# Kernel tuning notes

Measured on AMD Instinct MI355X. Metric: run time of the kernel, lower is better.

## Reference

```python
import jax, jax.numpy as jnp
import numpy as np

# Module constants from init_kwargs
DIM = 3      # qudit dimension
NQ = 15      # number of qudits
INDEX = 7    # target qudit -> esq = INDEX qudits left, dir = NQ-INDEX-1 right
J, K = 0, 1  # generalized sigma_x levels
D = DIM ** NQ


def setup_inputs() -> dict:
    key = jax.random.key(0)
    k1, k2, k3 = jax.random.split(key, 3)
    x_real = jax.random.normal(k1, (D, 1), dtype=jnp.float32)
    x_imag = jax.random.normal(k2, (D, 1), dtype=jnp.float32)
    angle = jax.random.normal(k3, (1,), dtype=jnp.float32)
    return {"x_real": x_real, "x_imag": x_imag, "angle": angle}


def reference(x_real, x_imag, angle):
    # Generator S = |j><k| + |k><j| (generalized sigma_x, mtx_id=0)
    S = jnp.zeros((DIM, DIM), dtype=jnp.complex64).at[J, K].set(1.0).at[K, J].set(1.0)
    # M = expm(-0.5i * angle * S), a tiny DIMxDIM unitary
    M = jax.scipy.linalg.expm((-0.5j) * angle[0].astype(jnp.complex64) * S)
    # State vector: complex amplitudes
    x = jax.lax.complex(x_real, x_imag)  # (D, 1) complex64
    d_left = DIM ** INDEX
    d_right = DIM ** (NQ - INDEX - 1)
    # (I_left kron M kron I_right) @ x == contract M on the middle qudit axis
    xr = x.reshape(d_left, DIM, d_right)
    y = jnp.einsum('ij,ajb->aib', M, xr)
    return y.reshape(D, 1)
```

## Files before the change

### kernel.cpp

```cpp
#include <hip/hip_runtime.h>
#include <hip/hip_bf16.h>


constexpr int DR = 2187;
constexpr int ROWSTRIDE = 3 * DR;
constexpr int NPAIRS = 4782969;

__global__ __launch_bounds__(256) void rot_kernel(
    const float* __restrict__ xr,
    const float* __restrict__ xi,
    const float* __restrict__ angle,
    __hip_bfloat162* __restrict__ out)
{
    int p = blockIdx.x * blockDim.x + threadIdx.x;
    if (p >= NPAIRS) return;

    float half = 0.5f * angle[0];
    float s = sinf(half);
    float c = cosf(half);

    int a = p / DR;
    int b = p - a * DR;
    int base = a * ROWSTRIDE + b;

    float x0r = xr[base],          x0i = xi[base];
    float x1r = xr[base + DR],     x1i = xi[base + DR];
    float x2r = xr[base + 2 * DR], x2i = xi[base + 2 * DR];

    float y0r = c * x0r + s * x1i;
    float y0i = c * x0i - s * x1r;
    float y1r = s * x0i + c * x1r;
    float y1i = c * x1i - s * x0r;

    __hip_bfloat162 o0, o1, o2;
    o0.x = __float2bfloat16(y0i); o0.y = __float2bfloat16(y0r);
    o1.x = __float2bfloat16(y1i); o1.y = __float2bfloat16(y1r);
    o2.x = __float2bfloat16(x2i); o2.y = __float2bfloat16(x2r);

    out[base]          = o0;
    out[base + DR]     = o1;
    out[base + 2 * DR] = o2;
}

extern "C" void kernel_launch(void* const* d_in, const int* in_sizes, int n_in,
                              void* d_out, int out_size, void* d_ws, size_t ws_size,
                              hipStream_t stream) {
    const float* big[2] = {nullptr, nullptr};
    const float* angle = nullptr;
    int nbig = 0;
    for (int i = 0; i < n_in; ++i) {
        if (in_sizes[i] == 1) angle = (const float*)d_in[i];
        else if (nbig < 2)    big[nbig++] = (const float*)d_in[i];
    }
    const float* xr = big[0];
    const float* xi = big[1];
    __hip_bfloat162* out = (__hip_bfloat162*)d_out;

    const int block = 256;
    const int grid = (NPAIRS + block - 1) / block;
    rot_kernel<<<grid, block, 0, stream>>>(xr, xi, angle, out);
}
```

Measured before the change: 32.74 us.

## Stage row planes in LDS with float4 loads and vectorize passthrough plane

Each block now handles one left index row: the first two qudit planes are loaded with float4 vector loads into shared memory, and the untouched third plane is copied straight to output with float4 loads and packed 128-bit stores. The rotation then reads partner elements from LDS. This replaces scalar strided per-thread loads and the per-element divide with wide coalesced transfers, at the cost of a block-wide barrier, about 35KB of LDS per block, and alignment prologue/epilogue handling.

```diff
diff --git a/kernel.cpp b/kernel.cpp
--- a/kernel.cpp
+++ b/kernel.cpp
@@ -2,44 +2,100 @@
 #include <hip/hip_bf16.h>
 
 
-constexpr int DR = 2187;
-constexpr int ROWSTRIDE = 3 * DR;
-constexpr int NPAIRS = 4782969;
+constexpr int PLANE = 2187;
+constexpr int TWO_PLANES = 4374;
+constexpr int ROWLEN = 6561;
+constexpr int NROWS = 2187;
 
-__global__ __launch_bounds__(256) void rot_kernel(
+__device__ __forceinline__ uint32_t pack_bf2(float re, float im) {
+    __hip_bfloat162 h;
+    h.x = __float2bfloat16(im);
+    h.y = __float2bfloat16(re);
+    return *reinterpret_cast<uint32_t*>(&h);
+}
+
+__global__ __launch_bounds__(256, 4) void rot_kernel(
     const float* __restrict__ xr,
     const float* __restrict__ xi,
     const float* __restrict__ angle,
-    __hip_bfloat162* __restrict__ out)
+    uint32_t* __restrict__ out)
 {
-    int p = blockIdx.x * blockDim.x + threadIdx.x;
-    if (p >= NPAIRS) return;
+    __shared__ __align__(16) float s_xr[TWO_PLANES + 6];
+    __shared__ __align__(16) float s_xi[TWO_PLANES + 6];
 
-    float half = 0.5f * angle[0];
-    float s = sinf(half);
-    float c = cosf(half);
+    const int tid = threadIdx.x;
+    const int a   = blockIdx.x;
+    const int g   = a * ROWLEN;
 
-    int a = p / DR;
-    int b = p - a * DR;
-    int base = a * ROWSTRIDE + b;
+    const float half = 0.5f * angle[0];
+    const float s = sinf(half);
+    const float c = cosf(half);
 
-    float x0r = xr[base],          x0i = xi[base];
-    float x1r = xr[base + DR],     x1i = xi[base + DR];
-    float x2r = xr[base + 2 * DR], x2i = xi[base + 2 * DR];
+    const int off = g & 3;
+    const int pre = (4 - off) & 3;
+    const int nq  = (TWO_PLANES - pre) >> 2;
+    if (tid < pre) {
+        s_xr[tid + off] = xr[g + tid];
+        s_xi[tid + off] = xi[g + tid];
+    }
+    const float4* gr = reinterpret_cast<const float4*>(xr + g + pre);
+    const float4* gi = reinterpret_cast<const float4*>(xi + g + pre);
+    float4* sr4 = reinterpret_cast<float4*>(&s_xr[pre + off]);
+    float4* si4 = reinterpret_cast<float4*>(&s_xi[pre + off]);
+    for (int q = tid; q < nq; q += 256) {
+        sr4[q] = gr[q];
+        si4[q] = gi[q];
+    }
+    {
+        int e = pre + 4 * nq + tid;
+        if (e < TWO_PLANES) {
+            s_xr[e + off] = xr[g + e];
+            s_xi[e + off] = xi[g + e];
+        }
+    }
 
-    float y0r = c * x0r + s * x1i;
-    float y0i = c * x0i - s * x1r;
-    float y1r = s * x0i + c * x1r;
-    float y1i = c * x1i - s * x0r;
+    {
+        const int g2   = g + TWO_PLANES;
+        const int pre2 = (4 - (g2 & 3)) & 3;
+        const int nq2  = (PLANE - pre2) >> 2;
+        if (tid < pre2) {
+            int idx = g2 + tid;
+            out[idx] = pack_bf2(xr[idx], xi[idx]);
+        }
+        const float4* gr2 = reinterpret_cast<const float4*>(xr + g2 + pre2);
+        const float4* gi2 = reinterpret_cast<const float4*>(xi + g2 + pre2);
+        uint4* o4 = reinterpret_cast<uint4*>(out + g2 + pre2);
+        for (int q = tid; q < nq2; q += 256) {
+            float4 r = gr2[q];
+            float4 i = gi2[q];
+            uint4 o;
+            o.x = pack_bf2(r.x, i.x);
+            o.y = pack_bf2(r.y, i.y);
+            o.z = pack_bf2(r.z, i.z);
+            o.w = pack_bf2(r.w, i.w);
+            o4[q] = o;
+        }
+        int e2 = pre2 + 4 * nq2 + tid;
+        if (e2 < PLANE) {
+            int idx = g2 + e2;
+            out[idx] = pack_bf2(xr[idx], xi[idx]);
+        }
+    }
 
-    __hip_bfloat162 o0, o1, o2;
-    o0.x = __float2bfloat16(y0i); o0.y = __float2bfloat16(y0r);
-    o1.x = __float2bfloat16(y1i); o1.y = __float2bfloat16(y1r);
-    o2.x = __float2bfloat16(x2i); o2.y = __float2bfloat16(x2r);
+    __syncthreads();
 
-    out[base]          = o0;
-    out[base + DR]     = o1;
-    out[base + 2 * DR] = o2;
+    #pragma unroll
+    for (int m = 0; m < 18; ++m) {
+        int e = tid + (m << 8);
+        if (e < TWO_PLANES) {
+            int p = e + ((e < PLANE) ? PLANE : -PLANE);
+            float xre = s_xr[e + off], xie = s_xi[e + off];
+            float xrp = s_xr[p + off], xip = s_xi[p + off];
+            float yr = c * xre + s * xip;
+            float yi = c * xie - s * xrp;
+            out[g + e] = pack_bf2(yr, yi);
+        }
+    }
 }
 
 extern "C" void kernel_launch(void* const* d_in, const int* in_sizes, int n_in,
@@ -54,9 +110,7 @@
     }
     const float* xr = big[0];
     const float* xi = big[1];
-    __hip_bfloat162* out = (__hip_bfloat162*)d_out;
+    uint32_t* out = (uint32_t*)d_out;
 
-    const int block = 256;
-    const int grid = (NPAIRS + block - 1) / block;
-    rot_kernel<<<grid, block, 0, stream>>>(xr, xi, angle, out);
+    rot_kernel<<<NROWS, 256, 0, stream>>>(xr, xi, angle, out);
 }
```

New measurement: 35.53 us. 8.5% more time.

## Vectorize rotation kernel to process four contiguous elements per thread

Applied to the files above, without the earlier changes.

Each thread now handles four consecutive state elements using float4 loads and a single 16-byte packed bf16 store. For the two rotated planes, partner values are gathered with unaligned-offset vector loads from the neighbouring plane. This replaces scalar strided accesses with wider transactions, but partner data is loaded a second time by a different thread, so it relies on cache to avoid extra DRAM traffic.

```diff
diff --git a/kernel.cpp b/kernel.cpp
--- a/kernel.cpp
+++ b/kernel.cpp
@@ -2,44 +2,83 @@
 #include <hip/hip_bf16.h>
 
 
-constexpr int DR = 2187;
-constexpr int ROWSTRIDE = 3 * DR;
-constexpr int NPAIRS = 4782969;
+constexpr int PLANE = 2187;
+constexpr int D     = 14348907;
+constexpr int NQUAD = (D + 3) >> 2;
+
+__device__ __forceinline__ uint32_t pack_bf2(float re, float im) {
+    __hip_bfloat162 h;
+    h.x = __float2bfloat16(im);
+    h.y = __float2bfloat16(re);
+    return *reinterpret_cast<uint32_t*>(&h);
+}
+
+__device__ __forceinline__ float4 ld4(const float* p) {
+    return *reinterpret_cast<const float4*>(p);
+}
 
 __global__ __launch_bounds__(256) void rot_kernel(
     const float* __restrict__ xr,
     const float* __restrict__ xi,
     const float* __restrict__ angle,
-    __hip_bfloat162* __restrict__ out)
+    uint32_t* __restrict__ out)
 {
-    int p = blockIdx.x * blockDim.x + threadIdx.x;
-    if (p >= NPAIRS) return;
+    const int q = blockIdx.x * blockDim.x + threadIdx.x;
+    if (q >= NQUAD) return;
+    const int e = q << 2;
 
-    float half = 0.5f * angle[0];
-    float s = sinf(half);
-    float c = cosf(half);
+    const float half = 0.5f * angle[0];
+    const float s = sinf(half);
+    const float c = cosf(half);
 
-    int a = p / DR;
-    int b = p - a * DR;
-    int base = a * ROWSTRIDE + b;
+    const int t = e / PLANE;
+    const int j = t % 3;
+    const int b = e - t * PLANE;
 
-    float x0r = xr[base],          x0i = xi[base];
-    float x1r = xr[base + DR],     x1i = xi[base + DR];
-    float x2r = xr[base + 2 * DR], x2i = xi[base + 2 * DR];
-
-    float y0r = c * x0r + s * x1i;
-    float y0i = c * x0i - s * x1r;
-    float y1r = s * x0i + c * x1r;
-    float y1i = c * x1i - s * x0r;
-
-    __hip_bfloat162 o0, o1, o2;
-    o0.x = __float2bfloat16(y0i); o0.y = __float2bfloat16(y0r);
-    o1.x = __float2bfloat16(y1i); o1.y = __float2bfloat16(y1r);
-    o2.x = __float2bfloat16(x2i); o2.y = __float2bfloat16(x2r);
-
-    out[base]          = o0;
-    out[base + DR]     = o1;
-    out[base + 2 * DR] = o2;
+    if (b + 3 < PLANE && e + 3 < D) {
+        const float4 sr = ld4(xr + e);
+        const float4 si = ld4(xi + e);
+        uint4 o;
+        if (j == 2) {
+            o.x = pack_bf2(sr.x, si.x); o.y = pack_bf2(sr.y, si.y);
+            o.z = pack_bf2(sr.z, si.z); o.w = pack_bf2(sr.w, si.w);
+        } else {
+            float pr0, pr1, pr2, pr3, pi0, pi1, pi2, pi3;
+            if (j == 0) {
+                const int pb = e + 2184;
+                float4 ar = ld4(xr + pb), br = ld4(xr + pb + 4);
+                float4 ai = ld4(xi + pb), bi = ld4(xi + pb + 4);
+                pr0 = ar.w; pr1 = br.x; pr2 = br.y; pr3 = br.z;
+                pi0 = ai.w; pi1 = bi.x; pi2 = bi.y; pi3 = bi.z;
+            } else {
+                const int pb = e - 2188;
+                float4 ar = ld4(xr + pb), br = ld4(xr + pb + 4);
+                float4 ai = ld4(xi + pb), bi = ld4(xi + pb + 4);
+                pr0 = ar.y; pr1 = ar.z; pr2 = ar.w; pr3 = br.x;
+                pi0 = ai.y; pi1 = ai.z; pi2 = ai.w; pi3 = bi.x;
+            }
+            o.x = pack_bf2(c * sr.x + s * pi0, c * si.x - s * pr0);
+            o.y = pack_bf2(c * sr.y + s * pi1, c * si.y - s * pr1);
+            o.z = pack_bf2(c * sr.z + s * pi2, c * si.z - s * pr2);
+            o.w = pack_bf2(c * sr.w + s * pi3, c * si.w - s * pr3);
+        }
+        *reinterpret_cast<uint4*>(out + e) = o;
+    } else {
+        #pragma unroll
+        for (int k = 0; k < 4; ++k) {
+            int e2 = e + k;
+            if (e2 >= D) break;
+            int t2 = e2 / PLANE;
+            int j2 = t2 % 3;
+            float r = xr[e2], i = xi[e2];
+            if (j2 == 2) {
+                out[e2] = pack_bf2(r, i);
+            } else {
+                int p = e2 + ((j2 == 0) ? PLANE : -PLANE);
+                out[e2] = pack_bf2(c * r + s * xi[p], c * i - s * xr[p]);
+            }
+        }
+    }
 }
 
 extern "C" void kernel_launch(void* const* d_in, const int* in_sizes, int n_in,
@@ -54,9 +93,9 @@
     }
     const float* xr = big[0];
     const float* xi = big[1];
-    __hip_bfloat162* out = (__hip_bfloat162*)d_out;
+    uint32_t* out = (uint32_t*)d_out;
 
     const int block = 256;
-    const int grid = (NPAIRS + block - 1) / block;
+    const int grid = (NQUAD + block - 1) / block;
     rot_kernel<<<grid, block, 0, stream>>>(xr, xi, angle, out);
 }
```

Measured after the change: 41.04 us. 25.4% more time.
